# Optimization experiments

Measured on AMD Instinct MI355X. Metric: run time of the kernel, lower is better.

Reference implementation:

```python
import jax, jax.numpy as jnp
import numpy as np

EMBED_DIM = 2048
NUM_HEADS = 32
HEAD_DIM = EMBED_DIM // NUM_HEADS
SCALE = HEAD_DIM ** -0.5
B, S = 2, 2048


def setup_inputs() -> dict:
    key = jax.random.key(0)
    ks = jax.random.split(key, 9)
    std = EMBED_DIM ** -0.5
    inp = {
        "h": jax.random.normal(ks[0], (B, S, EMBED_DIM), dtype=jnp.float32),
        "Wq": jax.random.normal(ks[1], (EMBED_DIM, EMBED_DIM), dtype=jnp.float32) * std,
        "bq": jax.random.normal(ks[2], (EMBED_DIM,), dtype=jnp.float32) * 0.02,
        "Wk": jax.random.normal(ks[3], (EMBED_DIM, EMBED_DIM), dtype=jnp.float32) * std,
        "bk": jax.random.normal(ks[4], (EMBED_DIM,), dtype=jnp.float32) * 0.02,
        "Wv": jax.random.normal(ks[5], (EMBED_DIM, EMBED_DIM), dtype=jnp.float32) * std,
        "bv": jax.random.normal(ks[6], (EMBED_DIM,), dtype=jnp.float32) * 0.02,
        "Wo": jax.random.normal(ks[7], (EMBED_DIM, EMBED_DIM), dtype=jnp.float32) * std,
        "bo": jax.random.normal(ks[8], (EMBED_DIM,), dtype=jnp.float32) * 0.02,
    }
    return inp


def reference(h, Wq, bq, Wk, bk, Wv, bv, Wo, bo):
    # QKV projections (nn.Linear: x @ W.T + b)
    q = h @ Wq.T + bq  # [B, S, E]
    k = h @ Wk.T + bk
    v = h @ Wv.T + bv
    # split heads
    q = q.reshape(B, S, NUM_HEADS, HEAD_DIM)
    k = k.reshape(B, S, NUM_HEADS, HEAD_DIM)
    v = v.reshape(B, S, NUM_HEADS, HEAD_DIM)
    # scaled dot-product attention with causal (tril) mask
    scores = jnp.einsum("bqhd,bkhd->bhqk", q, k) * SCALE  # [B, H, S, S]
    causal = jnp.tril(jnp.ones((S, S), dtype=bool))  # [S, S]
    neg = jnp.finfo(scores.dtype).min
    scores = jnp.where(causal[None, None, :, :], scores, neg)
    attn = jax.nn.softmax(scores, axis=-1)
    o = jnp.einsum("bhqk,bkhd->bqhd", attn, v).reshape(B, S, EMBED_DIM)
    return o @ Wo.T + bo
```

## Files before the change

kernel.cpp:

```cpp
#include <hip/hip_runtime.h>
#include <hip/hip_bf16.h>
#include <stdint.h>

#define EMBED 2048
#define NHEADS 32
#define HDIM 64
#define BATCH 2
#define SEQ 2048
#define ATT_SCALE 0.125f
#define LOG2E 1.4426950408889634f

typedef __attribute__((ext_vector_type(8))) short bf16x8;
typedef __attribute__((ext_vector_type(4))) float f32x4;
typedef __attribute__((ext_vector_type(16))) float f32x16;
typedef __attribute__((ext_vector_type(4))) unsigned short u16x4;
typedef __attribute__((ext_vector_type(2))) unsigned int u32x2;

static __device__ __forceinline__ unsigned short f2bf(float f) {
  union { float f; uint32_t u; } v; v.f = f;
  uint32_t r = v.u + 0x7fffu + ((v.u >> 16) & 1u);
  return (unsigned short)(r >> 16);
}

static __device__ __forceinline__ void gload_lds16(const unsigned short* g, unsigned short* l) {
  __builtin_amdgcn_global_load_lds(
      (const __attribute__((address_space(1))) unsigned int*)g,
      (__attribute__((address_space(3))) unsigned int*)l, 16, 0, 0);
}

__global__ void cvt_all(const float* __restrict__ h,
                        const float* __restrict__ Wq, const float* __restrict__ Wk,
                        const float* __restrict__ Wv, const float* __restrict__ Wo,
                        unsigned short* __restrict__ out) {
  const int n4 = 6291456;
  int idx = blockIdx.x * blockDim.x + threadIdx.x;
  int stride = gridDim.x * blockDim.x;
  for (int i = idx; i < n4; i += stride) {
    const float* src; int off;
    if (i < 2097152)      { src = h;  off = i; }
    else if (i < 3145728) { src = Wq; off = i - 2097152; }
    else if (i < 4194304) { src = Wk; off = i - 3145728; }
    else if (i < 5242880) { src = Wv; off = i - 4194304; }
    else                  { src = Wo; off = i - 5242880; }
    float4 v = ((const float4*)src)[off];
    u16x4 o;
    o.x = f2bf(v.x); o.y = f2bf(v.y); o.z = f2bf(v.z); o.w = f2bf(v.w);
    ((u16x4*)out)[i] = o;
  }
}

__global__ __launch_bounds__(512, 2)
void gemm256_qkv(const unsigned short* __restrict__ A,
                 const unsigned short* __restrict__ W,
                 const float* __restrict__ b0, const float* __restrict__ b1,
                 const float* __restrict__ b2,
                 unsigned short* __restrict__ o0, unsigned short* __restrict__ o1,
                 unsigned short* __restrict__ o2, float qscale) {
  __shared__ unsigned short lds[2][32768];
  const int tid = threadIdx.x;
  const int w = tid >> 6, l = tid & 63;
  const int wm = w >> 2, wn = w & 3;
  const int r16 = l & 15, g = l >> 4;
  const int xcd = blockIdx.x & 7, t8 = blockIdx.x >> 3;
  const int bi = (xcd >> 2) * 8 + (t8 & 7);
  const int bj = (xcd & 3) * 6 + (t8 >> 3);
  const int arow0 = bi * 256, bcol0 = bj * 256;

  f32x4 acc[8][4];
#pragma unroll
  for (int i = 0; i < 8; ++i)
#pragma unroll
    for (int j = 0; j < 4; ++j) acc[i][j] = (f32x4){0.f, 0.f, 0.f, 0.f};

  const int lr8 = (l >> 3) & 7;
  const int gcu = ((l & 7) ^ lr8) * 8;
  const int wb = (w & 3) * 8 + (w >> 2) * 64;

  auto stageA = [&](int buf, int kt, int base) {
    gload_lds16(A + (size_t)(arow0 + base + (tid >> 3)) * 2048 + kt * 64 + gcu,
                &lds[buf][(base + w * 8) * 64]);
  };
  auto stageB = [&](int buf, int kt, int nh, int k) {
    const int rbase = wb + nh * 32 + k * 128;
    gload_lds16(W + (size_t)(bcol0 + rbase + (l >> 3)) * 2048 + kt * 64 + gcu,
                &lds[buf][16384 + rbase * 64]);
  };
  auto ldA = [&](int buf, int mf, int ks) -> bf16x8 {
    const int row = wm * 128 + mf * 16 + r16;
    const int u = (ks * 4 + g) ^ (r16 & 7);
    return *(const bf16x8*)&lds[buf][row * 64 + u * 8];
  };
  auto ldB = [&](int buf, int nf, int ks) -> bf16x8 {
    const int row = wn * 64 + nf * 16 + r16;
    const int u = (ks * 4 + g) ^ (r16 & 7);
    return *(const bf16x8*)&lds[buf][16384 + row * 64 + u * 8];
  };

  bf16x8 af[4][2], bfr[4][2];

#define MMA_Q(MH, NH)                                                              \
  __builtin_amdgcn_s_setprio(1);                                                   \
  _Pragma("unroll")                                                                \
  for (int i = 0; i < 4; ++i)                                                      \
    _Pragma("unroll")                                                              \
    for (int j = 0; j < 2; ++j)                                                    \
      _Pragma("unroll")                                                            \
      for (int ks = 0; ks < 2; ++ks)                                               \
        acc[(MH)*4 + i][(NH)*2 + j] = __builtin_amdgcn_mfma_f32_16x16x32_bf16(     \
            af[i][ks], bfr[(NH)*2 + j][ks], acc[(MH)*4 + i][(NH)*2 + j], 0, 0, 0); \
  __builtin_amdgcn_s_setprio(0);

  stageB(0, 0, 0, 0); stageB(0, 0, 0, 1);
  stageB(0, 0, 1, 0); stageB(0, 0, 1, 1);
  stageA(0, 0, 0); stageA(0, 0, 128);
  stageA(0, 0, 64); stageA(0, 0, 192);
  asm volatile("s_waitcnt vmcnt(2)" ::: "memory");
  __builtin_amdgcn_sched_barrier(0);
  __builtin_amdgcn_s_barrier();

  const int nt = 32;
  for (int c = 0; c < nt; ++c) {
    const int X = c & 1, Y = X ^ 1;
    const bool s1 = (c + 1 < nt);
#pragma unroll
    for (int i = 0; i < 4; ++i) { af[i][0] = ldA(X, i, 0); af[i][1] = ldA(X, i, 1); }
#pragma unroll
    for (int j = 0; j < 2; ++j) { bfr[j][0] = ldB(X, j, 0); bfr[j][1] = ldB(X, j, 1); }
    if (s1) { stageB(Y, c + 1, 0, 0); stageB(Y, c + 1, 0, 1); }
    MMA_Q(0, 0);
    __builtin_amdgcn_s_barrier();
#pragma unroll
    for (int j = 2; j < 4; ++j) { bfr[j][0] = ldB(X, j, 0); bfr[j][1] = ldB(X, j, 1); }
    if (s1) { stageB(Y, c + 1, 1, 0); stageB(Y, c + 1, 1, 1); }
    MMA_Q(0, 1);
    __builtin_amdgcn_s_barrier();
    if (s1) asm volatile("s_waitcnt vmcnt(4)" ::: "memory");
    else    asm volatile("s_waitcnt vmcnt(0)" ::: "memory");
    __builtin_amdgcn_sched_barrier(0);
#pragma unroll
    for (int i = 0; i < 4; ++i) { af[i][0] = ldA(X, i + 4, 0); af[i][1] = ldA(X, i + 4, 1); }
    if (s1) { stageA(Y, c + 1, 0); stageA(Y, c + 1, 128); }
    MMA_Q(1, 0);
    __builtin_amdgcn_s_barrier();
    if (s1) { stageA(Y, c + 1, 64); stageA(Y, c + 1, 192); }
    MMA_Q(1, 1);
    if (s1) asm volatile("s_waitcnt vmcnt(2)" ::: "memory");
    else    asm volatile("s_waitcnt vmcnt(0)" ::: "memory");
    __builtin_amdgcn_sched_barrier(0);
    __builtin_amdgcn_s_barrier();
  }
#undef MMA_Q

  const int which = bj >> 3;
  const float* bb = (which == 0) ? b0 : (which == 1) ? b1 : b2;
  const float osc = (which == 0) ? qscale : 1.0f;
  unsigned short* outp = (which == 0) ? o0 : (which == 1) ? o1 : o2;
#pragma unroll
  for (int mf = 0; mf < 8; ++mf) {
    const int irow = arow0 + wm * 128 + mf * 16 + g * 4;
#pragma unroll
    for (int nf = 0; nf < 4; ++nf) {
      const int jcol = bcol0 + wn * 64 + nf * 16 + r16;
      const int jl = jcol & 2047;
      const int hh = jl >> 6, d = jl & 63;
      const float bval = bb[jl];
#pragma unroll
      for (int rr = 0; rr < 4; ++rr) {
        const float val = (acc[mf][nf][rr] + bval) * osc;
        const int i = irow + rr;
        const int b = i >> 11, s = i & 2047;
        size_t off;
        if (which < 2) off = (((size_t)(b * NHEADS + hh)) * SEQ + s) * HDIM + d;
        else           off = (((size_t)(b * NHEADS + hh)) * HDIM + d) * SEQ + s;
        outp[off] = f2bf(val);
      }
    }
  }
}

__global__ __launch_bounds__(512, 2)
void gemm8_out(const unsigned short* __restrict__ A,
               const unsigned short* __restrict__ W,
               const float* __restrict__ bias, float* __restrict__ fo) {
  __shared__ unsigned short lds[2][24576];
  const int tid = threadIdx.x;
  const int w = tid >> 6, l = tid & 63;
  const int wm = w >> 1, wn = w & 1;
  const int r16 = l & 15, g = l >> 4;
  const int NBJ = 16, nblk = 256;
  const int swz = (blockIdx.x & 7) * (nblk >> 3) + (blockIdx.x >> 3);
  const int bi = swz / NBJ, bj = swz % NBJ;
  const int arow0 = bi * 256, bcol0 = bj * 128;

  f32x4 acc[4][4];
#pragma unroll
  for (int i = 0; i < 4; ++i)
#pragma unroll
    for (int j = 0; j < 4; ++j) acc[i][j] = (f32x4){0.f, 0.f, 0.f, 0.f};

  const int lrow = l >> 3;
  const int gcu = ((l & 7) ^ lrow) * 8;

  auto stageA = [&](int buf, int t, int mq, int call) {
    const int m = call * 8 + w;
    const int row0 = mq * 32 + (m >> 2) * 64 + (m & 3) * 8;
    gload_lds16(A + (size_t)(arow0 + row0 + lrow) * 2048 + t * 64 + gcu,
                &lds[buf][row0 * 64]);
  };
  auto stageB = [&](int buf, int t, int nq) {
    const int row0 = nq * 32 + (w >> 2) * 64 + (w & 3) * 8;
    gload_lds16(W + (size_t)(bcol0 + row0 + lrow) * 2048 + t * 64 + gcu,
                &lds[buf][16384 + row0 * 64]);
  };
  auto ldA = [&](int buf, int mf, int ks) -> bf16x8 {
    const int row = wm * 64 + mf * 16 + r16;
    const int u = (ks * 4 + g) ^ (r16 & 7);
    return *(const bf16x8*)&lds[buf][row * 64 + u * 8];
  };
  auto ldB = [&](int buf, int nf, int ks) -> bf16x8 {
    const int row = wn * 64 + nf * 16 + r16;
    const int u = (ks * 4 + g) ^ (r16 & 7);
    return *(const bf16x8*)&lds[buf][16384 + row * 64 + u * 8];
  };

  stageA(0, 0, 0, 0); stageA(0, 0, 0, 1); stageB(0, 0, 0);
  stageA(0, 0, 1, 0); stageA(0, 0, 1, 1); stageB(0, 0, 1);
  stageA(1, 1, 0, 0); stageA(1, 1, 0, 1); stageB(1, 1, 0);
  asm volatile("s_waitcnt vmcnt(3)" ::: "memory");
  __builtin_amdgcn_sched_barrier(0);
  __builtin_amdgcn_s_barrier();

  bf16x8 af[2][2], bfr[4][2];

#define MMA_Q(MQ, NQ)                                                          \
  __builtin_amdgcn_s_setprio(1);                                               \
  _Pragma("unroll")                                                            \
  for (int i = 0; i < 2; ++i)                                                  \
    _Pragma("unroll")                                                          \
    for (int j = 0; j < 2; ++j)                                                \
      _Pragma("unroll")                                                        \
      for (int ks = 0; ks < 2; ++ks)                                           \
        acc[(MQ)*2 + i][(NQ)*2 + j] = __builtin_amdgcn_mfma_f32_16x16x32_bf16( \
            af[i][ks], bfr[(NQ)*2 + j][ks], acc[(MQ)*2 + i][(NQ)*2 + j], 0, 0, 0); \
  __builtin_amdgcn_s_setprio(0);

  const int nt = 32;
  for (int c = 0; c < nt; ++c) {
    const int X = c & 1;
    const bool s1 = (c + 1 < nt), s2 = (c + 2 < nt);
    af[0][0] = ldA(X, 0, 0); af[0][1] = ldA(X, 0, 1);
    af[1][0] = ldA(X, 1, 0); af[1][1] = ldA(X, 1, 1);
    bfr[0][0] = ldB(X, 0, 0); bfr[0][1] = ldB(X, 0, 1);
    bfr[1][0] = ldB(X, 1, 0); bfr[1][1] = ldB(X, 1, 1);
    if (s1) { stageA(X ^ 1, c + 1, 1, 0); stageA(X ^ 1, c + 1, 1, 1); }
    MMA_Q(0, 0);
    __builtin_amdgcn_s_barrier();
    bfr[2][0] = ldB(X, 2, 0); bfr[2][1] = ldB(X, 2, 1);
    bfr[3][0] = ldB(X, 3, 0); bfr[3][1] = ldB(X, 3, 1);
    if (s1) stageB(X ^ 1, c + 1, 1);
    MMA_Q(0, 1);
    __builtin_amdgcn_s_barrier();
    af[0][0] = ldA(X, 2, 0); af[0][1] = ldA(X, 2, 1);
    af[1][0] = ldA(X, 3, 0); af[1][1] = ldA(X, 3, 1);
    if (s2) { stageA(X, c + 2, 0, 0); stageA(X, c + 2, 0, 1); }
    MMA_Q(1, 0);
    __builtin_amdgcn_s_barrier();
    if (s2) stageB(X, c + 2, 0);
    MMA_Q(1, 1);
    if (s2) asm volatile("s_waitcnt vmcnt(3)" ::: "memory");
    else    asm volatile("s_waitcnt vmcnt(0)" ::: "memory");
    __builtin_amdgcn_sched_barrier(0);
    __builtin_amdgcn_s_barrier();
  }
#undef MMA_Q

#pragma unroll
  for (int mf = 0; mf < 4; ++mf) {
    const int irow = arow0 + wm * 64 + mf * 16 + g * 4;
#pragma unroll
    for (int nf = 0; nf < 4; ++nf) {
      const int jcol = bcol0 + wn * 64 + nf * 16 + r16;
      const float bval = bias[jcol];
#pragma unroll
      for (int rr = 0; rr < 4; ++rr)
        fo[(size_t)(irow + rr) * 2048 + jcol] = acc[mf][nf][rr] + bval;
    }
  }
}

__global__ __launch_bounds__(256, 2)
void attn_kernel(const unsigned short* __restrict__ Q,
                 const unsigned short* __restrict__ K,
                 const unsigned short* __restrict__ Vt,
                 unsigned short* __restrict__ O) {
  __shared__ unsigned short K_lds[2][64 * 72];
  __shared__ unsigned short V_lds[2][64 * 72];
  __shared__ __align__(16) float abuf[4][32];
  __shared__ __align__(16) float lbuf[4][32];
  const int tid = threadIdx.x;
  const int w = tid >> 6, l = tid & 63;
  const int q5 = l & 31, hi = l >> 5;
  const int bid = ((blockIdx.x & 7) << 6) | (blockIdx.x >> 3);
  const int pair = bid & 7;
  const int bh = bid >> 3;
  const unsigned short* Qh = Q + (size_t)bh * SEQ * HDIM;
  const unsigned short* Kh = K + (size_t)bh * SEQ * HDIM;
  const unsigned short* Vh = Vt + (size_t)bh * HDIM * SEQ;
  const int bq = bh >> 5, hh = bh & 31;
  const int srow = tid >> 3;
  const int scol = (tid & 7) * 8;

  for (int half = 0; half < 2; ++half) {
    const int qt = half ? (15 - pair) : pair;
    const int wrow0 = qt * 128 + w * 32;
    const int wrow_max = wrow0 + 31;
    const int n_tiles = 2 * qt + 2;
    const int qrow = wrow0 + q5;

    bf16x8 qf[4];
#pragma unroll
    for (int ks = 0; ks < 4; ++ks)
      qf[ks] = *(const bf16x8*)(Qh + (size_t)qrow * HDIM + ks * 16 + hi * 8);

    f32x16 oacc[2];
#pragma unroll
    for (int df = 0; df < 2; ++df)
#pragma unroll
      for (int r = 0; r < 16; ++r) oacc[df][r] = 0.f;
    float m_run = -3.0e38f, l_run = 0.f;

    bf16x8 kreg[2], vreg[2];
#pragma unroll
    for (int j = 0; j < 2; ++j) {
      const int rr = j * 32 + srow;
      kreg[j] = *(const bf16x8*)(Kh + (size_t)rr * HDIM + scol);
      vreg[j] = *(const bf16x8*)(Vh + (size_t)rr * SEQ + scol);
    }
    __syncthreads();
#pragma unroll
    for (int j = 0; j < 2; ++j) {
      const int rr = j * 32 + srow;
      *(bf16x8*)(K_lds[0] + rr * 72 + scol) = kreg[j];
      *(bf16x8*)(V_lds[0] + rr * 72 + scol) = vreg[j];
    }

    for (int t = 0; t < n_tiles; ++t) {
      const int cur = t & 1;
      const bool not_last = (t + 1 < n_tiles);
      if (not_last) {
#pragma unroll
        for (int j = 0; j < 2; ++j) {
          const int rr = j * 32 + srow;
          kreg[j] = *(const bf16x8*)(Kh + (size_t)((t + 1) * 64 + rr) * HDIM + scol);
          vreg[j] = *(const bf16x8*)(Vh + (size_t)rr * SEQ + (t + 1) * 64 + scol);
        }
      }
      __syncthreads();

      if (t * 64 <= wrow_max) {
        f32x16 skf[2];
#pragma unroll
        for (int kf = 0; kf < 2; ++kf)
#pragma unroll
          for (int r = 0; r < 16; ++r) skf[kf][r] = 0.f;
        __builtin_amdgcn_s_setprio(1);
#pragma unroll
        for (int kf = 0; kf < 2; ++kf)
#pragma unroll
          for (int ks = 0; ks < 4; ++ks) {
            bf16x8 ak = *(const bf16x8*)(K_lds[cur] + (kf * 32 + q5) * 72 + ks * 16 + hi * 8);
            skf[kf] = __builtin_amdgcn_mfma_f32_32x32x16_bf16(ak, qf[ks], skf[kf], 0, 0, 0);
          }
        __builtin_amdgcn_s_setprio(0);

        const bool need_mask = (t * 64 + 63 > wrow0);
        if (need_mask) {
#pragma unroll
          for (int kf = 0; kf < 2; ++kf)
#pragma unroll
            for (int r = 0; r < 16; ++r) {
              const int key = t * 64 + kf * 32 + (r & 3) + 8 * (r >> 2) + 4 * hi;
              if (key > qrow) skf[kf][r] = -3.0e38f;
            }
        }

        float mx = -3.0e38f;
#pragma unroll
        for (int kf = 0; kf < 2; ++kf)
#pragma unroll
          for (int r = 0; r < 16; ++r) mx = fmaxf(mx, skf[kf][r]);
        mx = fmaxf(mx, __shfl_xor(mx, 32));

        if (__any(mx > m_run + 8.0f)) {
          const float mnew = fmaxf(m_run, mx);
          const float alpha = exp2f(m_run - mnew);
          m_run = mnew;
          l_run *= alpha;
          if (l < 32) abuf[w][l] = alpha;
          f32x4 av[4];
#pragma unroll
          for (int k = 0; k < 4; ++k)
            av[k] = *(const f32x4*)&abuf[w][8 * k + 4 * hi];
#pragma unroll
          for (int df = 0; df < 2; ++df)
#pragma unroll
            for (int r = 0; r < 16; ++r) oacc[df][r] *= av[r >> 2][r & 3];
        }

        unsigned int pkA[8], pkB[8];
        float psum = 0.f;
#pragma unroll
        for (int kf = 0; kf < 2; ++kf)
#pragma unroll
          for (int rr = 0; rr < 4; ++rr) {
            unsigned int pb[4];
#pragma unroll
            for (int j = 0; j < 4; ++j) {
              const float p = exp2f(skf[kf][rr * 4 + j] - m_run);
              psum += p;
              union { float f; unsigned int u; } c; c.f = p;
              pb[j] = c.u + 0x8000u;
            }
            pkA[kf * 4 + rr] = __builtin_amdgcn_perm(pb[1], pb[0], 0x07060302);
            pkB[kf * 4 + rr] = __builtin_amdgcn_perm(pb[3], pb[2], 0x07060302);
          }
        psum += __shfl_xor(psum, 32);
        l_run += psum;

        __builtin_amdgcn_s_setprio(1);
#pragma unroll
        for (int ks = 0; ks < 4; ++ks) {
          u32x2 ra = __builtin_amdgcn_permlane32_swap(pkA[2 * ks], pkA[2 * ks + 1], false, false);
          u32x2 rb = __builtin_amdgcn_permlane32_swap(pkB[2 * ks], pkB[2 * ks + 1], false, false);
          union { unsigned int u[4]; bf16x8 v; } pa;
          pa.u[0] = ra.x; pa.u[1] = rb.x; pa.u[2] = ra.y; pa.u[3] = rb.y;
#pragma unroll
          for (int df = 0; df < 2; ++df) {
            bf16x8 vf = *(const bf16x8*)(V_lds[cur] + (df * 32 + q5) * 72 + ks * 16 + hi * 8);
            oacc[df] = __builtin_amdgcn_mfma_f32_32x32x16_bf16(pa.v, vf, oacc[df], 0, 0, 0);
          }
        }
        __builtin_amdgcn_s_setprio(0);
      }

      if (not_last) {
#pragma unroll
        for (int j = 0; j < 2; ++j) {
          const int rr = j * 32 + srow;
          *(bf16x8*)(K_lds[cur ^ 1] + rr * 72 + scol) = kreg[j];
          *(bf16x8*)(V_lds[cur ^ 1] + rr * 72 + scol) = vreg[j];
        }
      }
    }

    if (l < 32) lbuf[w][l] = l_run;
    f32x4 lv[4];
#pragma unroll
    for (int k = 0; k < 4; ++k)
      lv[k] = *(const f32x4*)&lbuf[w][8 * k + 4 * hi];
#pragma unroll
    for (int df = 0; df < 2; ++df) {
      const int d = df * 32 + q5;
#pragma unroll
      for (int r = 0; r < 16; ++r) {
        const int s = wrow0 + (r & 3) + 8 * (r >> 2) + 4 * hi;
        const float inv = __builtin_amdgcn_rcpf(lv[r >> 2][r & 3]);
        O[((size_t)(bq * SEQ + s)) * EMBED + hh * HDIM + d] = f2bf(oacc[df][r] * inv);
      }
    }
  }
}

extern "C" void kernel_launch(void* const* d_in, const int* in_sizes, int n_in,
                              void* d_out, int out_size, void* d_ws, size_t ws_size,
                              hipStream_t stream) {
  const float* h  = (const float*)d_in[0];
  const float* Wq = (const float*)d_in[1];
  const float* bq = (const float*)d_in[2];
  const float* Wk = (const float*)d_in[3];
  const float* bk = (const float*)d_in[4];
  const float* Wv = (const float*)d_in[5];
  const float* bv = (const float*)d_in[6];
  const float* Wo = (const float*)d_in[7];
  const float* bo = (const float*)d_in[8];

  if (ws_size < (size_t)117440512) return;

  unsigned short* ws = (unsigned short*)d_ws;
  unsigned short* hb = ws;
  unsigned short* wqb = ws + 8388608;
  unsigned short* wob = ws + 20971520;
  unsigned short* Qw  = ws + 25165824;
  unsigned short* Kw  = ws + 33554432;
  unsigned short* Vw  = ws + 41943040;
  unsigned short* Ow  = ws + 50331648;

  cvt_all<<<2048, 256, 0, stream>>>(h, Wq, Wk, Wv, Wo, ws);

  const float qscale = ATT_SCALE * LOG2E;
  gemm256_qkv<<<384, 512, 0, stream>>>(hb, wqb, bq, bk, bv, Qw, Kw, Vw, qscale);

  attn_kernel<<<512, 256, 0, stream>>>(Qw, Kw, Vw, Ow);

  gemm8_out<<<256, 512, 0, stream>>>(Ow, wob, bo, (float*)d_out);
}
```

Baseline: 276.1 us.

## Restructure QKV GEMM into 8-phase ping-pong pipeline with interleaved warp tiles

Rewrites the main loop of the fused QKV projection GEMM. It processes two K-tiles per iteration across eight barrier-delimited MMA phases and prefetches tile t+2 while computing t and t+1, with vmcnt(6) waits. The warp-to-output mapping changes so each warp owns interleaved 64x32 quadrants instead of one contiguous 128x64 block, and the A/B reuse order alternates. This aims to overlap global-to-LDS staging with MFMA work in the HipKittens 8-wave style, at the cost of more barriers and tighter wait-count bookkeeping.

```diff
diff --git a/kernel.cpp b/kernel.cpp
--- a/kernel.cpp
+++ b/kernel.cpp
@@ -63,7 +63,7 @@
   const int r16 = l & 15, g = l >> 4;
   const int xcd = blockIdx.x & 7, t8 = blockIdx.x >> 3;
   const int bi = (xcd >> 2) * 8 + (t8 & 7);
-  const int bj = (xcd & 3) * 6 + (t8 >> 3);
+  const int bj = (xcd & 3) * 6 + (t8 / 8);
   const int arow0 = bi * 256, bcol0 = bj * 256;
 
   f32x4 acc[8][4];
@@ -72,110 +72,132 @@
 #pragma unroll
     for (int j = 0; j < 4; ++j) acc[i][j] = (f32x4){0.f, 0.f, 0.f, 0.f};
 
-  const int lr8 = (l >> 3) & 7;
-  const int gcu = ((l & 7) ^ lr8) * 8;
-  const int wb = (w & 3) * 8 + (w >> 2) * 64;
-
-  auto stageA = [&](int buf, int kt, int base) {
-    gload_lds16(A + (size_t)(arow0 + base + (tid >> 3)) * 2048 + kt * 64 + gcu,
-                &lds[buf][(base + w * 8) * 64]);
-  };
-  auto stageB = [&](int buf, int kt, int nh, int k) {
-    const int rbase = wb + nh * 32 + k * 128;
-    gload_lds16(W + (size_t)(bcol0 + rbase + (l >> 3)) * 2048 + kt * 64 + gcu,
-                &lds[buf][16384 + rbase * 64]);
-  };
-  auto ldA = [&](int buf, int mf, int ks) -> bf16x8 {
-    const int row = wm * 128 + mf * 16 + r16;
+  const int gcu = ((l & 7) ^ ((l >> 3) & 7)) * 8;
+
+  auto stA = [&](int buf, int t, int grp) {
+    gload_lds16(A + (size_t)(arow0 + grp * 64 + (tid >> 3)) * 2048 + t * 64 + gcu,
+                &lds[buf][(grp * 64 + w * 8) * 64]);
+  };
+  auto stB = [&](int buf, int t, int grp) {
+    gload_lds16(W + (size_t)(bcol0 + grp * 64 + (tid >> 3)) * 2048 + t * 64 + gcu,
+                &lds[buf][16384 + (grp * 64 + w * 8) * 64]);
+  };
+  auto ldA = [&](int buf, int mq, int mf, int ks) -> bf16x8 {
+    const int row = mq * 128 + wm * 64 + mf * 16 + r16;
     const int u = (ks * 4 + g) ^ (r16 & 7);
     return *(const bf16x8*)&lds[buf][row * 64 + u * 8];
   };
-  auto ldB = [&](int buf, int nf, int ks) -> bf16x8 {
-    const int row = wn * 64 + nf * 16 + r16;
+  auto ldB = [&](int buf, int nq, int nf, int ks) -> bf16x8 {
+    const int row = nq * 128 + wn * 32 + nf * 16 + r16;
     const int u = (ks * 4 + g) ^ (r16 & 7);
     return *(const bf16x8*)&lds[buf][16384 + row * 64 + u * 8];
   };
 
-  bf16x8 af[4][2], bfr[4][2];
-
-#define MMA_Q(MH, NH)                                                              \
-  __builtin_amdgcn_s_setprio(1);                                                   \
-  _Pragma("unroll")                                                                \
-  for (int i = 0; i < 4; ++i)                                                      \
-    _Pragma("unroll")                                                              \
-    for (int j = 0; j < 2; ++j)                                                    \
-      _Pragma("unroll")                                                            \
-      for (int ks = 0; ks < 2; ++ks)                                               \
-        acc[(MH)*4 + i][(NH)*2 + j] = __builtin_amdgcn_mfma_f32_16x16x32_bf16(     \
-            af[i][ks], bfr[(NH)*2 + j][ks], acc[(MH)*4 + i][(NH)*2 + j], 0, 0, 0); \
+  bf16x8 af[4][2], bq0[2][2], bq1[2][2];
+
+#define MMAQ(MQ, NQ, BF)                                                       \
+  __builtin_amdgcn_s_setprio(1);                                               \
+  _Pragma("unroll")                                                            \
+  for (int mf = 0; mf < 4; ++mf)                                               \
+    _Pragma("unroll")                                                          \
+    for (int nf = 0; nf < 2; ++nf)                                             \
+      _Pragma("unroll")                                                        \
+      for (int ks = 0; ks < 2; ++ks)                                           \
+        acc[(MQ)*4 + mf][(NQ)*2 + nf] = __builtin_amdgcn_mfma_f32_16x16x32_bf16( \
+            af[mf][ks], BF[nf][ks], acc[(MQ)*4 + mf][(NQ)*2 + nf], 0, 0, 0);   \
   __builtin_amdgcn_s_setprio(0);
 
-  stageB(0, 0, 0, 0); stageB(0, 0, 0, 1);
-  stageB(0, 0, 1, 0); stageB(0, 0, 1, 1);
-  stageA(0, 0, 0); stageA(0, 0, 128);
-  stageA(0, 0, 64); stageA(0, 0, 192);
-  asm volatile("s_waitcnt vmcnt(2)" ::: "memory");
-  __builtin_amdgcn_sched_barrier(0);
+#define PH_OPEN()                                          \
+  __builtin_amdgcn_s_barrier();                            \
+  asm volatile("s_waitcnt lgkmcnt(0)" ::: "memory");       \
+  __builtin_amdgcn_sched_barrier(0)
+#define PH_CLOSE() __builtin_amdgcn_s_barrier()
+#define VMC6() { asm volatile("s_waitcnt vmcnt(6)" ::: "memory"); __builtin_amdgcn_sched_barrier(0); }
+#define VMC0() { asm volatile("s_waitcnt vmcnt(0)" ::: "memory"); __builtin_amdgcn_sched_barrier(0); }
+
+  stA(0, 0, 0); stA(0, 0, 1); stB(0, 0, 0); stB(0, 0, 1);
+  stB(0, 0, 2); stB(0, 0, 3); stA(0, 0, 2); stA(0, 0, 3);
+  stA(1, 1, 0); stA(1, 1, 1); stB(1, 1, 0); stB(1, 1, 1);
+  stB(1, 1, 2); stB(1, 1, 3);
+  VMC6();
   __builtin_amdgcn_s_barrier();
 
-  const int nt = 32;
-  for (int c = 0; c < nt; ++c) {
-    const int X = c & 1, Y = X ^ 1;
-    const bool s1 = (c + 1 < nt);
-#pragma unroll
-    for (int i = 0; i < 4; ++i) { af[i][0] = ldA(X, i, 0); af[i][1] = ldA(X, i, 1); }
-#pragma unroll
-    for (int j = 0; j < 2; ++j) { bfr[j][0] = ldB(X, j, 0); bfr[j][1] = ldB(X, j, 1); }
-    if (s1) { stageB(Y, c + 1, 0, 0); stageB(Y, c + 1, 0, 1); }
-    MMA_Q(0, 0);
-    __builtin_amdgcn_s_barrier();
-#pragma unroll
-    for (int j = 2; j < 4; ++j) { bfr[j][0] = ldB(X, j, 0); bfr[j][1] = ldB(X, j, 1); }
-    if (s1) { stageB(Y, c + 1, 1, 0); stageB(Y, c + 1, 1, 1); }
-    MMA_Q(0, 1);
-    __builtin_amdgcn_s_barrier();
-    if (s1) asm volatile("s_waitcnt vmcnt(4)" ::: "memory");
-    else    asm volatile("s_waitcnt vmcnt(0)" ::: "memory");
-    __builtin_amdgcn_sched_barrier(0);
-#pragma unroll
-    for (int i = 0; i < 4; ++i) { af[i][0] = ldA(X, i + 4, 0); af[i][1] = ldA(X, i + 4, 1); }
-    if (s1) { stageA(Y, c + 1, 0); stageA(Y, c + 1, 128); }
-    MMA_Q(1, 0);
-    __builtin_amdgcn_s_barrier();
-    if (s1) { stageA(Y, c + 1, 64); stageA(Y, c + 1, 192); }
-    MMA_Q(1, 1);
-    if (s1) asm volatile("s_waitcnt vmcnt(2)" ::: "memory");
-    else    asm volatile("s_waitcnt vmcnt(0)" ::: "memory");
-    __builtin_amdgcn_sched_barrier(0);
-    __builtin_amdgcn_s_barrier();
+  const int nit = 16;
+  for (int j = 0; j < nit; ++j) {
+    const int t0 = 2 * j, t1 = t0 + 1;
+    const bool sf = (j + 1 < nit);
+#pragma unroll
+    for (int mf = 0; mf < 4; ++mf) { af[mf][0] = ldA(0, 0, mf, 0); af[mf][1] = ldA(0, 0, mf, 1); }
+#pragma unroll
+    for (int nf = 0; nf < 2; ++nf) { bq0[nf][0] = ldB(0, 0, nf, 0); bq0[nf][1] = ldB(0, 0, nf, 1); }
+    stA(1, t1, 2); stA(1, t1, 3);
+    PH_OPEN(); MMAQ(0, 0, bq0); PH_CLOSE();
+#pragma unroll
+    for (int nf = 0; nf < 2; ++nf) { bq1[nf][0] = ldB(0, 1, nf, 0); bq1[nf][1] = ldB(0, 1, nf, 1); }
+    if (sf) { stA(0, t0 + 2, 0); stA(0, t0 + 2, 1); }
+    PH_OPEN(); MMAQ(0, 1, bq1); PH_CLOSE();
+#pragma unroll
+    for (int mf = 0; mf < 4; ++mf) { af[mf][0] = ldA(0, 1, mf, 0); af[mf][1] = ldA(0, 1, mf, 1); }
+    if (sf) { stB(0, t0 + 2, 0); stB(0, t0 + 2, 1); }
+    PH_OPEN(); MMAQ(1, 1, bq1); PH_CLOSE();
+    if (sf) { stB(0, t0 + 2, 2); stB(0, t0 + 2, 3); }
+    PH_OPEN(); MMAQ(1, 0, bq0);
+    if (sf) VMC6() else VMC0();
+    PH_CLOSE();
+#pragma unroll
+    for (int mf = 0; mf < 4; ++mf) { af[mf][0] = ldA(1, 0, mf, 0); af[mf][1] = ldA(1, 0, mf, 1); }
+#pragma unroll
+    for (int nf = 0; nf < 2; ++nf) { bq0[nf][0] = ldB(1, 0, nf, 0); bq0[nf][1] = ldB(1, 0, nf, 1); }
+    if (sf) { stA(0, t0 + 2, 2); stA(0, t0 + 2, 3); }
+    PH_OPEN(); MMAQ(0, 0, bq0); PH_CLOSE();
+#pragma unroll
+    for (int nf = 0; nf < 2; ++nf) { bq1[nf][0] = ldB(1, 1, nf, 0); bq1[nf][1] = ldB(1, 1, nf, 1); }
+    if (sf) { stA(1, t1 + 2, 0); stA(1, t1 + 2, 1); }
+    PH_OPEN(); MMAQ(0, 1, bq1); PH_CLOSE();
+#pragma unroll
+    for (int mf = 0; mf < 4; ++mf) { af[mf][0] = ldA(1, 1, mf, 0); af[mf][1] = ldA(1, 1, mf, 1); }
+    if (sf) { stB(1, t1 + 2, 0); stB(1, t1 + 2, 1); }
+    PH_OPEN(); MMAQ(1, 1, bq1); PH_CLOSE();
+    if (sf) { stB(1, t1 + 2, 2); stB(1, t1 + 2, 3); }
+    PH_OPEN(); MMAQ(1, 0, bq0);
+    if (sf) VMC6() else VMC0();
+    PH_CLOSE();
   }
-#undef MMA_Q
+#undef MMAQ
+#undef PH_OPEN
+#undef PH_CLOSE
+#undef VMC6
+#undef VMC0
 
   const int which = bj >> 3;
   const float* bb = (which == 0) ? b0 : (which == 1) ? b1 : b2;
   const float osc = (which == 0) ? qscale : 1.0f;
   unsigned short* outp = (which == 0) ? o0 : (which == 1) ? o1 : o2;
 #pragma unroll
-  for (int mf = 0; mf < 8; ++mf) {
-    const int irow = arow0 + wm * 128 + mf * 16 + g * 4;
-#pragma unroll
-    for (int nf = 0; nf < 4; ++nf) {
-      const int jcol = bcol0 + wn * 64 + nf * 16 + r16;
-      const int jl = jcol & 2047;
-      const int hh = jl >> 6, d = jl & 63;
-      const float bval = bb[jl];
-#pragma unroll
-      for (int rr = 0; rr < 4; ++rr) {
-        const float val = (acc[mf][nf][rr] + bval) * osc;
-        const int i = irow + rr;
-        const int b = i >> 11, s = i & 2047;
-        size_t off;
-        if (which < 2) off = (((size_t)(b * NHEADS + hh)) * SEQ + s) * HDIM + d;
-        else           off = (((size_t)(b * NHEADS + hh)) * HDIM + d) * SEQ + s;
-        outp[off] = f2bf(val);
-      }
+  for (int mq = 0; mq < 2; ++mq)
+#pragma unroll
+    for (int mf = 0; mf < 4; ++mf) {
+      const int irow = arow0 + mq * 128 + wm * 64 + mf * 16 + g * 4;
+#pragma unroll
+      for (int nq = 0; nq < 2; ++nq)
+#pragma unroll
+        for (int nf = 0; nf < 2; ++nf) {
+          const int jcol = bcol0 + nq * 128 + wn * 32 + nf * 16 + r16;
+          const int jl = jcol & 2047;
+          const int hh = jl >> 6, d = jl & 63;
+          const float bval = bb[jl];
+#pragma unroll
+          for (int rr = 0; rr < 4; ++rr) {
+            const float val = (acc[mq * 4 + mf][nq * 2 + nf][rr] + bval) * osc;
+            const int i = irow + rr;
+            const int b = i >> 11, s = i & 2047;
+            size_t off;
+            if (which < 2) off = (((size_t)(b * NHEADS + hh)) * SEQ + s) * HDIM + d;
+            else           off = (((size_t)(b * NHEADS + hh)) * HDIM + d) * SEQ + s;
+            outp[off] = f2bf(val);
+          }
+        }
     }
-  }
 }
 
 __global__ __launch_bounds__(512, 2)
```

Result: no change. 280.8 us (+1.7%).

## Shrink QKV GEMM tile to 256x128 with single-buffered B for more occupancy

Applied to the files above, without the earlier changes.

The QKV projection GEMM moves from 256x256 tiles to 256x128 tiles, which doubles the grid to 768 blocks. It keeps double-buffered A in LDS but holds B in a single buffer that is reloaded after its last use in each iteration. LDS per block drops, and launch bounds rise to 4 blocks per CU to improve occupancy and wave balance across CUs. In exchange, each A tile is read twice as often from global memory, and a full vmcnt(0) wait every iteration removes some load/compute overlap.

```diff
diff --git a/kernel.cpp b/kernel.cpp
--- a/kernel.cpp
+++ b/kernel.cpp
@@ -49,115 +49,111 @@
   }
 }
 
-__global__ __launch_bounds__(512, 2)
-void gemm256_qkv(const unsigned short* __restrict__ A,
+__global__ __launch_bounds__(512, 4)
+void gemm_qkv_sb(const unsigned short* __restrict__ A,
                  const unsigned short* __restrict__ W,
                  const float* __restrict__ b0, const float* __restrict__ b1,
                  const float* __restrict__ b2,
                  unsigned short* __restrict__ o0, unsigned short* __restrict__ o1,
                  unsigned short* __restrict__ o2, float qscale) {
-  __shared__ unsigned short lds[2][32768];
+  __shared__ unsigned short ldsA[2][16384];
+  __shared__ unsigned short ldsB[8192];
   const int tid = threadIdx.x;
   const int w = tid >> 6, l = tid & 63;
-  const int wm = w >> 2, wn = w & 3;
+  const int wm = w >> 1, wn = w & 1;
   const int r16 = l & 15, g = l >> 4;
   const int xcd = blockIdx.x & 7, t8 = blockIdx.x >> 3;
   const int bi = (xcd >> 2) * 8 + (t8 & 7);
-  const int bj = (xcd & 3) * 6 + (t8 >> 3);
-  const int arow0 = bi * 256, bcol0 = bj * 256;
-
-  f32x4 acc[8][4];
-#pragma unroll
-  for (int i = 0; i < 8; ++i)
+  const int bj = (xcd & 3) * 12 + (t8 >> 3);
+  const int arow0 = bi * 256, bcol0 = bj * 128;
+
+  f32x4 acc[4][4];
+#pragma unroll
+  for (int i = 0; i < 4; ++i)
 #pragma unroll
     for (int j = 0; j < 4; ++j) acc[i][j] = (f32x4){0.f, 0.f, 0.f, 0.f};
 
-  const int lr8 = (l >> 3) & 7;
-  const int gcu = ((l & 7) ^ lr8) * 8;
-  const int wb = (w & 3) * 8 + (w >> 2) * 64;
-
-  auto stageA = [&](int buf, int kt, int base) {
-    gload_lds16(A + (size_t)(arow0 + base + (tid >> 3)) * 2048 + kt * 64 + gcu,
-                &lds[buf][(base + w * 8) * 64]);
-  };
-  auto stageB = [&](int buf, int kt, int nh, int k) {
-    const int rbase = wb + nh * 32 + k * 128;
-    gload_lds16(W + (size_t)(bcol0 + rbase + (l >> 3)) * 2048 + kt * 64 + gcu,
-                &lds[buf][16384 + rbase * 64]);
+  const int lrow = l >> 3;
+  const int gcu = ((l & 7) ^ lrow) * 8;
+
+  auto stageA = [&](int buf, int t, int mq, int call) {
+    const int m = call * 8 + w;
+    const int row0 = mq * 32 + (m >> 2) * 64 + (m & 3) * 8;
+    gload_lds16(A + (size_t)(arow0 + row0 + lrow) * 2048 + t * 64 + gcu,
+                &ldsA[buf][row0 * 64]);
+  };
+  auto stageB = [&](int t, int nq) {
+    const int row0 = nq * 32 + (w >> 2) * 64 + (w & 3) * 8;
+    gload_lds16(W + (size_t)(bcol0 + row0 + lrow) * 2048 + t * 64 + gcu,
+                &ldsB[row0 * 64]);
   };
   auto ldA = [&](int buf, int mf, int ks) -> bf16x8 {
-    const int row = wm * 128 + mf * 16 + r16;
+    const int row = wm * 64 + mf * 16 + r16;
     const int u = (ks * 4 + g) ^ (r16 & 7);
-    return *(const bf16x8*)&lds[buf][row * 64 + u * 8];
-  };
-  auto ldB = [&](int buf, int nf, int ks) -> bf16x8 {
+    return *(const bf16x8*)&ldsA[buf][row * 64 + u * 8];
+  };
+  auto ldB = [&](int nf, int ks) -> bf16x8 {
     const int row = wn * 64 + nf * 16 + r16;
     const int u = (ks * 4 + g) ^ (r16 & 7);
-    return *(const bf16x8*)&lds[buf][16384 + row * 64 + u * 8];
-  };
-
-  bf16x8 af[4][2], bfr[4][2];
-
-#define MMA_Q(MH, NH)                                                              \
-  __builtin_amdgcn_s_setprio(1);                                                   \
-  _Pragma("unroll")                                                                \
-  for (int i = 0; i < 4; ++i)                                                      \
-    _Pragma("unroll")                                                              \
-    for (int j = 0; j < 2; ++j)                                                    \
-      _Pragma("unroll")                                                            \
-      for (int ks = 0; ks < 2; ++ks)                                               \
-        acc[(MH)*4 + i][(NH)*2 + j] = __builtin_amdgcn_mfma_f32_16x16x32_bf16(     \
-            af[i][ks], bfr[(NH)*2 + j][ks], acc[(MH)*4 + i][(NH)*2 + j], 0, 0, 0); \
+    return *(const bf16x8*)&ldsB[row * 64 + u * 8];
+  };
+
+  bf16x8 af[2][2], bfr[4][2];
+
+#define MMA_Q(MQ, NQ)                                                          \
+  __builtin_amdgcn_s_setprio(1);                                               \
+  _Pragma("unroll")                                                            \
+  for (int i = 0; i < 2; ++i)                                                  \
+    _Pragma("unroll")                                                          \
+    for (int j = 0; j < 2; ++j)                                                \
+      _Pragma("unroll")                                                        \
+      for (int ks = 0; ks < 2; ++ks)                                           \
+        acc[(MQ)*2 + i][(NQ)*2 + j] = __builtin_amdgcn_mfma_f32_16x16x32_bf16( \
+            af[i][ks], bfr[(NQ)*2 + j][ks], acc[(MQ)*2 + i][(NQ)*2 + j], 0, 0, 0); \
   __builtin_amdgcn_s_setprio(0);
 
-  stageB(0, 0, 0, 0); stageB(0, 0, 0, 1);
-  stageB(0, 0, 1, 0); stageB(0, 0, 1, 1);
-  stageA(0, 0, 0); stageA(0, 0, 128);
-  stageA(0, 0, 64); stageA(0, 0, 192);
-  asm volatile("s_waitcnt vmcnt(2)" ::: "memory");
+  stageA(0, 0, 0, 0); stageA(0, 0, 0, 1);
+  stageA(0, 0, 1, 0); stageA(0, 0, 1, 1);
+  stageB(0, 0); stageB(0, 1);
+  asm volatile("s_waitcnt vmcnt(0)" ::: "memory");
   __builtin_amdgcn_sched_barrier(0);
   __builtin_amdgcn_s_barrier();
 
   const int nt = 32;
   for (int c = 0; c < nt; ++c) {
-    const int X = c & 1, Y = X ^ 1;
+    const int X = c & 1;
     const bool s1 = (c + 1 < nt);
-#pragma unroll
-    for (int i = 0; i < 4; ++i) { af[i][0] = ldA(X, i, 0); af[i][1] = ldA(X, i, 1); }
-#pragma unroll
-    for (int j = 0; j < 2; ++j) { bfr[j][0] = ldB(X, j, 0); bfr[j][1] = ldB(X, j, 1); }
-    if (s1) { stageB(Y, c + 1, 0, 0); stageB(Y, c + 1, 0, 1); }
+    af[0][0] = ldA(X, 0, 0); af[0][1] = ldA(X, 0, 1);
+    af[1][0] = ldA(X, 1, 0); af[1][1] = ldA(X, 1, 1);
+    bfr[0][0] = ldB(0, 0); bfr[0][1] = ldB(0, 1);
+    bfr[1][0] = ldB(1, 0); bfr[1][1] = ldB(1, 1);
+    if (s1) { stageA(X ^ 1, c + 1, 1, 0); stageA(X ^ 1, c + 1, 1, 1); }
     MMA_Q(0, 0);
     __builtin_amdgcn_s_barrier();
-#pragma unroll
-    for (int j = 2; j < 4; ++j) { bfr[j][0] = ldB(X, j, 0); bfr[j][1] = ldB(X, j, 1); }
-    if (s1) { stageB(Y, c + 1, 1, 0); stageB(Y, c + 1, 1, 1); }
+    bfr[2][0] = ldB(2, 0); bfr[2][1] = ldB(2, 1);
+    bfr[3][0] = ldB(3, 0); bfr[3][1] = ldB(3, 1);
+    if (s1) { stageA(X ^ 1, c + 1, 0, 0); stageA(X ^ 1, c + 1, 0, 1); }
     MMA_Q(0, 1);
     __builtin_amdgcn_s_barrier();
-    if (s1) asm volatile("s_waitcnt vmcnt(4)" ::: "memory");
-    else    asm volatile("s_waitcnt vmcnt(0)" ::: "memory");
-    __builtin_amdgcn_sched_barrier(0);
-#pragma unroll
-    for (int i = 0; i < 4; ++i) { af[i][0] = ldA(X, i + 4, 0); af[i][1] = ldA(X, i + 4, 1); }
-    if (s1) { stageA(Y, c + 1, 0); stageA(Y, c + 1, 128); }
+    af[0][0] = ldA(X, 2, 0); af[0][1] = ldA(X, 2, 1);
+    af[1][0] = ldA(X, 3, 0); af[1][1] = ldA(X, 3, 1);
+    if (s1) { stageB(c + 1, 0); stageB(c + 1, 1); }
     MMA_Q(1, 0);
     __builtin_amdgcn_s_barrier();
-    if (s1) { stageA(Y, c + 1, 64); stageA(Y, c + 1, 192); }
     MMA_Q(1, 1);
-    if (s1) asm volatile("s_waitcnt vmcnt(2)" ::: "memory");
-    else    asm volatile("s_waitcnt vmcnt(0)" ::: "memory");
+    asm volatile("s_waitcnt vmcnt(0)" ::: "memory");
     __builtin_amdgcn_sched_barrier(0);
     __builtin_amdgcn_s_barrier();
   }
 #undef MMA_Q
 
-  const int which = bj >> 3;
+  const int which = bj >> 4;
   const float* bb = (which == 0) ? b0 : (which == 1) ? b1 : b2;
   const float osc = (which == 0) ? qscale : 1.0f;
   unsigned short* outp = (which == 0) ? o0 : (which == 1) ? o1 : o2;
 #pragma unroll
-  for (int mf = 0; mf < 8; ++mf) {
-    const int irow = arow0 + wm * 128 + mf * 16 + g * 4;
+  for (int mf = 0; mf < 4; ++mf) {
+    const int irow = arow0 + wm * 64 + mf * 16 + g * 4;
 #pragma unroll
     for (int nf = 0; nf < 4; ++nf) {
       const int jcol = bcol0 + wn * 64 + nf * 16 + r16;
@@ -498,7 +494,7 @@
   cvt_all<<<2048, 256, 0, stream>>>(h, Wq, Wk, Wv, Wo, ws);
 
   const float qscale = ATT_SCALE * LOG2E;
-  gemm256_qkv<<<384, 512, 0, stream>>>(hb, wqb, bq, bk, bv, Qw, Kw, Vw, qscale);
+  gemm_qkv_sb<<<768, 512, 0, stream>>>(hb, wqb, bq, bk, bv, Qw, Kw, Vw, qscale);
 
   attn_kernel<<<512, 256, 0, stream>>>(Qw, Kw, Vw, Ow);
 
```

After: 297.1 us. 1.08x slower.
